# Performance work log

Hardware: AMD Instinct MI355X
Metric: run time of the kernel (lower is better)

The kernel has to match this reference:

```python
import jax, jax.numpy as jnp
import numpy as np

N_NODES = 100000
N_EDGES = 1600000
IN_FEATS = 128
HIDDEN = 128
OUT_FEATS = 64
N_GRAPHS = 64


def setup_inputs() -> dict:
    key = jax.random.key(0)
    ks = jax.random.split(key, 12)
    features = jax.random.normal(ks[0], (N_NODES, IN_FEATS), dtype=jnp.float32)
    src = jax.random.randint(ks[1], (N_EDGES,), 0, N_NODES, dtype=jnp.int32)
    dst = jax.random.randint(ks[2], (N_EDGES,), 0, N_NODES, dtype=jnp.int32)
    graph_ids = jnp.sort(jax.random.randint(ks[3], (N_NODES,), 0, N_GRAPHS, dtype=jnp.int32))
    s = 0.05
    W1 = jax.random.normal(ks[4], (IN_FEATS, HIDDEN), dtype=jnp.float32) * s
    b1 = jnp.zeros((HIDDEN,), jnp.float32)
    W2 = jax.random.normal(ks[5], (HIDDEN, HIDDEN), dtype=jnp.float32) * s
    b2 = jnp.zeros((HIDDEN,), jnp.float32)
    Wd1 = jax.random.normal(ks[6], (HIDDEN, HIDDEN), dtype=jnp.float32) * s
    bd1 = jnp.zeros((HIDDEN,), jnp.float32)
    Wd2 = jax.random.normal(ks[7], (HIDDEN, OUT_FEATS), dtype=jnp.float32) * s
    bd2 = jnp.zeros((OUT_FEATS,), jnp.float32)
    return {"features": features, "src": src, "dst": dst, "graph_ids": graph_ids,
            "W1": W1, "b1": b1, "W2": W2, "b2": b2,
            "Wd1": Wd1, "bd1": bd1, "Wd2": Wd2, "bd2": bd2}


def _gin_conv(x, src, dst, W, b):
    # DGL GINConv(aggregator='mean', eps=0): h = Linear((1+eps)*x + mean_{u->v} x_u)
    agg_sum = jax.ops.segment_sum(x[src], dst, num_segments=N_NODES)  # [N, d]
    deg = jax.ops.segment_sum(jnp.ones((src.shape[0],), x.dtype), dst, num_segments=N_NODES)  # [N]
    agg = jnp.where(deg[:, None] > 0, agg_sum / jnp.maximum(deg, 1.0)[:, None], 0.0)
    return (x + agg) @ W + b


def reference(features, src, dst, graph_ids, W1, b1, W2, b2, Wd1, bd1, Wd2, bd2):
    h = jax.nn.relu(_gin_conv(features, src, dst, W1, b1))
    h = jax.nn.relu(_gin_conv(h, src, dst, W2, b2))
    # dgl.mean_nodes: per-graph mean over nodes
    hg_sum = jax.ops.segment_sum(h, graph_ids, num_segments=N_GRAPHS)  # [G, H]
    counts = jax.ops.segment_sum(jnp.ones((h.shape[0],), h.dtype), graph_ids, num_segments=N_GRAPHS)
    hg = hg_sum / jnp.maximum(counts, 1.0)[:, None]
    reconstructed = jax.nn.relu(hg @ Wd1 + bd1) @ Wd2 + bd2
    return (hg, reconstructed)
```

## Files before the change

### kernel.cpp

```cpp
#include <hip/hip_runtime.h>

#define NN 100000
#define NE 1600000
#define FD 128
#define NG 64
#define OUTD 64
#define NBIN 391

typedef __attribute__((ext_vector_type(8))) short bf16x8;
typedef __attribute__((ext_vector_type(4))) float f32x4;
typedef __attribute__((ext_vector_type(2))) float f32x2;
typedef __attribute__((ext_vector_type(8))) unsigned short u16x8;

static __device__ __forceinline__ void atomAddF(float* p, float v) {
    __hip_atomic_fetch_add(p, v, __ATOMIC_RELAXED, __HIP_MEMORY_SCOPE_AGENT);
}
static __device__ __forceinline__ int atomAddI(int* p, int v) {
    return __hip_atomic_fetch_add(p, v, __ATOMIC_RELAXED, __HIP_MEMORY_SCOPE_AGENT);
}
static __device__ __forceinline__ unsigned short f2bf(float f) {
    unsigned int u = __float_as_uint(f);
    u += 0x7FFFu + ((u >> 16) & 1u);
    return (unsigned short)(u >> 16);
}
static __device__ __forceinline__ float bf2f(unsigned short h) {
    return __uint_as_float(((unsigned int)h) << 16);
}
static __device__ __forceinline__ unsigned char f2fp8(float v) {
    return (unsigned char)(__builtin_amdgcn_cvt_pk_fp8_f32(v, v, 0, false) & 0xff);
}

__global__ __launch_bounds__(256) void k_pre(
    const int* __restrict__ dst, const int* __restrict__ gid,
    int* __restrict__ bincnt, float* __restrict__ gcount,
    const float* __restrict__ W1, const float* __restrict__ W2,
    unsigned short* __restrict__ W1t, unsigned short* __restrict__ W2t,
    unsigned int* __restrict__ Y8dummy, unsigned int* __restrict__ Y82dummy)
{
    const int t = threadIdx.x;
    if (blockIdx.x < NBIN) {
        __shared__ int h[NBIN];
        for (int i = t; i < NBIN; i += 256) h[i] = 0;
        __syncthreads();
        int e0 = blockIdx.x * 4096;
        int e1 = min(e0 + 4096, NE);
        for (int e = e0 + t; e < e1; e += 256)
            atomicAdd(&h[dst[e] >> 8], 1);
        __syncthreads();
        for (int i = t; i < NBIN; i += 256)
            if (h[i]) atomAddI(&bincnt[i], h[i]);
    } else if (blockIdx.x < 2 * NBIN) {
        __shared__ float c[NG];
        if (t < NG) c[t] = 0.0f;
        __syncthreads();
        int i = (blockIdx.x - NBIN) * 256 + t;
        if (i < NN) atomicAdd(&c[gid[i]], 1.0f);
        __syncthreads();
        if (t < NG) {
            float v = c[t];
            if (v != 0.0f) atomAddF(&gcount[t], v);
        }
    } else {
        int idx = (blockIdx.x - 2 * NBIN) * 256 + t;
        if (idx < 32768) {
            const float* W = (idx < 16384) ? W1 : W2;
            unsigned short* Wt = (idx < 16384) ? W1t : W2t;
            int i = idx & 16383;
            int k = i >> 7, n = i & 127;
            Wt[n * 128 + k] = f2bf(W[i]);
        } else if (idx < 32768 + 32) {
            Y8dummy[idx - 32768] = 0;
        } else if (idx < 32768 + 64) {
            Y82dummy[idx - 32768 - 32] = 0;
        }
    }
}

__global__ void k_boff(const int* __restrict__ bincnt, int* __restrict__ pstart,
                       int* __restrict__ bcur) {
    __shared__ int s[512];
    int t = threadIdx.x;
    int v = (t < NBIN) ? bincnt[t] : 0;
    s[t] = v;
    __syncthreads();
    for (int d = 1; d < 512; d <<= 1) {
        int x = (t >= d) ? s[t - d] : 0;
        __syncthreads();
        s[t] += x;
        __syncthreads();
    }
    if (t < NBIN) {
        int p = s[t] - v;
        pstart[t] = p;
        bcur[t * 16] = p;
    }
}

static __device__ __forceinline__ void gemm_body(
    int base, const float* __restrict__ feat, const unsigned short* __restrict__ Wt,
    unsigned char* __restrict__ Y8)
{
    const int lane = threadIdx.x & 63;
    const int w = threadIdx.x >> 6;
    const int r = lane & 15;
    const int kb = lane >> 4;
    const int row = base + w * 16 + r;
    const bool rok = row < NN;

    bf16x8 a[4];
    #pragma unroll
    for (int kt = 0; kt < 4; ++kt) {
        float4 lo = {0,0,0,0}, hi = {0,0,0,0};
        if (rok) {
            const float4* p = reinterpret_cast<const float4*>(
                feat + (size_t)row * FD + kt * 32 + kb * 8);
            lo = p[0]; hi = p[1];
        }
        bf16x8 t;
        t[0] = (short)f2bf(lo.x); t[1] = (short)f2bf(lo.y);
        t[2] = (short)f2bf(lo.z); t[3] = (short)f2bf(lo.w);
        t[4] = (short)f2bf(hi.x); t[5] = (short)f2bf(hi.y);
        t[6] = (short)f2bf(hi.z); t[7] = (short)f2bf(hi.w);
        a[kt] = t;
    }

    f32x4 acc[8];
    #pragma unroll
    for (int ct = 0; ct < 8; ++ct) acc[ct] = (f32x4){0.f, 0.f, 0.f, 0.f};

    const int n = lane & 15;
    #pragma unroll
    for (int ct = 0; ct < 8; ++ct) {
        int col = ct * 16 + n;
        #pragma unroll
        for (int kt = 0; kt < 4; ++kt) {
            bf16x8 b = *reinterpret_cast<const bf16x8*>(
                Wt + (size_t)col * FD + kt * 32 + kb * 8);
            acc[ct] = __builtin_amdgcn_mfma_f32_16x16x32_bf16(a[kt], b, acc[ct], 0, 0, 0);
        }
    }

    const int rbase = base + w * 16 + (lane >> 4) * 4;
    #pragma unroll
    for (int reg = 0; reg < 4; ++reg) {
        int node = rbase + reg;
        if (node < NN) {
            #pragma unroll
            for (int ct = 0; ct < 8; ++ct)
                Y8[(size_t)node * FD + ct * 16 + n] = f2fp8(acc[ct][reg]);
        }
    }
}

__global__ __launch_bounds__(256) void k_mix(
    const int* __restrict__ src, const int* __restrict__ dst,
    int* __restrict__ bcur, unsigned int* __restrict__ pbuf,
    const float* __restrict__ feat, const unsigned short* __restrict__ Wt,
    unsigned char* __restrict__ Y8)
{
    int g = blockIdx.x;
    if (g % 5 == 0) {
        gemm_body((g / 5) * 64, feat, Wt, Y8);
    } else {
        int fb = g - g / 5 - 1;
        int e = fb * 256 + threadIdx.x;
        if (e < NE) {
            int d = dst[e];
            int b = d >> 8;
            int p = atomAddI(&bcur[b * 16], 1);
            pbuf[p] = ((unsigned int)(d & 255) << 17) | (unsigned int)src[e];
        }
    }
}

__global__ __launch_bounds__(256) void k_fill2(
    const unsigned int* __restrict__ pbuf, const int* __restrict__ pstart,
    const int* __restrict__ bcur, int* __restrict__ degi, int* __restrict__ off,
    int* __restrict__ eidx)
{
    __shared__ int ldeg[256], lpre[256], lcur[256];
    const int b = blockIdx.x;
    const int t = threadIdx.x;
    const int st = pstart[b];
    const int en = bcur[b * 16];
    const int cnt = en - st;

    ldeg[t] = 0;
    __syncthreads();
    for (int i = t; i < cnt; i += 256)
        atomicAdd(&ldeg[(int)(pbuf[st + i] >> 17)], 1);
    __syncthreads();

    const int d = ldeg[t];
    const int rd = (d + 7) & ~7;
    lpre[t] = rd;
    __syncthreads();
    for (int dd = 1; dd < 256; dd <<= 1) {
        int x = (t >= dd) ? lpre[t - dd] : 0;
        __syncthreads();
        lpre[t] += x;
        __syncthreads();
    }

    const int ebase = st + b * 2048;
    const int o = ebase + lpre[t] - rd;
    const int v = (b << 8) + t;
    if (v < NN) {
        degi[v] = d;
        off[v] = o;
        for (int j = d; j < rd; ++j) eidx[o + j] = NN;
    }
    lcur[t] = o;
    __syncthreads();

    for (int i = t; i < cnt; i += 256) {
        unsigned int pk = pbuf[st + i];
        int dl = (int)(pk >> 17);
        int s  = (int)(pk & 0x1FFFF);
        int p = atomicAdd(&lcur[dl], 1);
        eidx[p] = s;
    }
}

__global__ __launch_bounds__(256) void k_aggmm(
    const unsigned char* __restrict__ Y8, const int* __restrict__ off,
    const int* __restrict__ degi, const int* __restrict__ eidx,
    const float* __restrict__ bias, const unsigned short* __restrict__ Wt2,
    unsigned char* __restrict__ Y82)
{
    __shared__ unsigned short At[16 * FD];
    const int t = blockIdx.x * 256 + threadIdx.x;
    const int v = t >> 4;
    const int l = threadIdx.x & 15;
    const int gb = threadIdx.x & 48;
    const int e0 = off[v];
    const int d  = degi[v];
    const int pd = (d + 7) & ~7;

    float a[8];
    #pragma unroll
    for (int j = 0; j < 8; ++j) a[j] = 0.0f;

    const uint2* Y8v = reinterpret_cast<const uint2*>(Y8);
    const int eend = e0 + pd;
    for (int e = e0; e < eend; e += 8) {
        int myidx = eidx[e + (l & 7)];
        #pragma unroll
        for (int j = 0; j < 8; ++j) {
            int s = __shfl(myidx, gb + j, 64);
            uint2 q = Y8v[(size_t)s * 16 + l];
            f32x2 v0 = __builtin_amdgcn_cvt_pk_f32_fp8((int)q.x, false);
            f32x2 v1 = __builtin_amdgcn_cvt_pk_f32_fp8((int)q.x, true);
            f32x2 v2 = __builtin_amdgcn_cvt_pk_f32_fp8((int)q.y, false);
            f32x2 v3 = __builtin_amdgcn_cvt_pk_f32_fp8((int)q.y, true);
            a[0] += v0[0]; a[1] += v0[1]; a[2] += v1[0]; a[3] += v1[1];
            a[4] += v2[0]; a[5] += v2[1]; a[6] += v3[0]; a[7] += v3[1];
        }
    }

    const float inv = 1.0f / fmaxf((float)d, 1.0f);
    uint2 qs = Y8v[(size_t)v * 16 + l];
    f32x2 s0 = __builtin_amdgcn_cvt_pk_f32_fp8((int)qs.x, false);
    f32x2 s1 = __builtin_amdgcn_cvt_pk_f32_fp8((int)qs.x, true);
    f32x2 s2 = __builtin_amdgcn_cvt_pk_f32_fp8((int)qs.y, false);
    f32x2 s3 = __builtin_amdgcn_cvt_pk_f32_fp8((int)qs.y, true);
    float sf[8] = { s0[0], s0[1], s1[0], s1[1], s2[0], s2[1], s3[0], s3[1] };
    const float4* bp = reinterpret_cast<const float4*>(bias + l * 8);
    float4 b0 = bp[0], b1 = bp[1];
    const float* bb[8] = { &b0.x, &b0.y, &b0.z, &b0.w, &b1.x, &b1.y, &b1.z, &b1.w };

    {
        u16x8 o;
        #pragma unroll
        for (int j = 0; j < 8; ++j)
            o[j] = f2bf(fmaxf(sf[j] + a[j] * inv + *bb[j], 0.0f));
        int g = threadIdx.x >> 4;
        char* AtB = reinterpret_cast<char*>(At);
        *reinterpret_cast<u16x8*>(AtB + g * 256 + ((l * 16) ^ ((g & 7) << 4))) = o;
    }
    __syncthreads();

    {
        const int lane = threadIdx.x & 63;
        const int w = threadIdx.x >> 6;
        const int r = lane & 15;
        const int kb = lane >> 4;
        const int n = lane & 15;
        char* AtB = reinterpret_cast<char*>(At);

        bf16x8 af[4];
        #pragma unroll
        for (int kt = 0; kt < 4; ++kt)
            af[kt] = *reinterpret_cast<bf16x8*>(
                AtB + r * 256 + ((kt * 64 + kb * 16) ^ ((r & 7) << 4)));

        f32x4 acc[2];
        acc[0] = (f32x4){0.f, 0.f, 0.f, 0.f};
        acc[1] = (f32x4){0.f, 0.f, 0.f, 0.f};
        #pragma unroll
        for (int ct = 0; ct < 2; ++ct) {
            int col = w * 32 + ct * 16 + n;
            #pragma unroll
            for (int kt = 0; kt < 4; ++kt) {
                bf16x8 bf = *reinterpret_cast<const bf16x8*>(
                    Wt2 + (size_t)col * FD + kt * 32 + kb * 8);
                acc[ct] = __builtin_amdgcn_mfma_f32_16x16x32_bf16(af[kt], bf, acc[ct], 0, 0, 0);
            }
        }

        const int nb = blockIdx.x * 16 + (lane >> 4) * 4;
        #pragma unroll
        for (int reg = 0; reg < 4; ++reg) {
            #pragma unroll
            for (int ct = 0; ct < 2; ++ct)
                Y82[(size_t)(nb + reg) * FD + w * 32 + ct * 16 + n] = f2fp8(acc[ct][reg]);
        }
    }
}

__global__ __launch_bounds__(256) void k_aggp(
    const unsigned char* __restrict__ Y82, const int* __restrict__ off,
    const int* __restrict__ degi, const int* __restrict__ eidx,
    const float* __restrict__ bias,
    const int* __restrict__ gid, float* __restrict__ hg_sum)
{
    __shared__ float hl[FD];
    if (threadIdx.x < FD) hl[threadIdx.x] = 0.0f;
    int gid0 = gid[blockIdx.x * 16];
    __syncthreads();

    const int t = blockIdx.x * 256 + threadIdx.x;
    const int v = t >> 4;
    const int l = threadIdx.x & 15;
    const int gb = threadIdx.x & 48;
    const int e0 = off[v];
    const int d  = degi[v];
    const int pd = (d + 7) & ~7;

    float a[8];
    #pragma unroll
    for (int j = 0; j < 8; ++j) a[j] = 0.0f;

    const uint2* Y8v = reinterpret_cast<const uint2*>(Y82);
    const int eend = e0 + pd;
    for (int e = e0; e < eend; e += 8) {
        int myidx = eidx[e + (l & 7)];
        #pragma unroll
        for (int j = 0; j < 8; ++j) {
            int s = __shfl(myidx, gb + j, 64);
            uint2 q = Y8v[(size_t)s * 16 + l];
            f32x2 v0 = __builtin_amdgcn_cvt_pk_f32_fp8((int)q.x, false);
            f32x2 v1 = __builtin_amdgcn_cvt_pk_f32_fp8((int)q.x, true);
            f32x2 v2 = __builtin_amdgcn_cvt_pk_f32_fp8((int)q.y, false);
            f32x2 v3 = __builtin_amdgcn_cvt_pk_f32_fp8((int)q.y, true);
            a[0] += v0[0]; a[1] += v0[1]; a[2] += v1[0]; a[3] += v1[1];
            a[4] += v2[0]; a[5] += v2[1]; a[6] += v3[0]; a[7] += v3[1];
        }
    }

    const float inv = 1.0f / fmaxf((float)d, 1.0f);
    uint2 qs = Y8v[(size_t)v * 16 + l];
    f32x2 s0 = __builtin_amdgcn_cvt_pk_f32_fp8((int)qs.x, false);
    f32x2 s1 = __builtin_amdgcn_cvt_pk_f32_fp8((int)qs.x, true);
    f32x2 s2 = __builtin_amdgcn_cvt_pk_f32_fp8((int)qs.y, false);
    f32x2 s3 = __builtin_amdgcn_cvt_pk_f32_fp8((int)qs.y, true);
    float sf[8] = { s0[0], s0[1], s1[0], s1[1], s2[0], s2[1], s3[0], s3[1] };
    const float4* bp = reinterpret_cast<const float4*>(bias + l * 8);
    float4 b0 = bp[0], b1 = bp[1];
    const float* bb[8] = { &b0.x, &b0.y, &b0.z, &b0.w, &b1.x, &b1.y, &b1.z, &b1.w };

    float hv[8];
    #pragma unroll
    for (int j = 0; j < 8; ++j)
        hv[j] = fmaxf(sf[j] + a[j] * inv + *bb[j], 0.0f);

    int g = gid[v];
    int fo = l * 8;
    if (g == gid0) {
        #pragma unroll
        for (int j = 0; j < 8; ++j) atomicAdd(&hl[fo + j], hv[j]);
    } else {
        #pragma unroll
        for (int j = 0; j < 8; ++j) atomAddF(&hg_sum[(size_t)g * FD + fo + j], hv[j]);
    }
    __syncthreads();
    if (threadIdx.x < FD)
        atomAddF(&hg_sum[(size_t)gid0 * FD + threadIdx.x], hl[threadIdx.x]);
}

__global__ __launch_bounds__(128) void k_dec(
    const float* __restrict__ hg_sum, const float* __restrict__ gcount,
    const float* __restrict__ Wd1, const float* __restrict__ bd1,
    const float* __restrict__ Wd2, const float* __restrict__ bd2,
    float* __restrict__ out)
{
    __shared__ float hgL[FD];
    __shared__ float t1L[FD];
    const int g = blockIdx.x;
    const int t = threadIdx.x;
    const float invc = 1.0f / fmaxf(gcount[g], 1.0f);

    float v = hg_sum[(size_t)g * FD + t] * invc;
    hgL[t] = v;
    out[(size_t)g * FD + t] = v;
    __syncthreads();

    float acc = bd1[t];
    #pragma unroll 8
    for (int k = 0; k < FD; ++k)
        acc += hgL[k] * Wd1[k * FD + t];
    t1L[t] = fmaxf(acc, 0.0f);
    __syncthreads();

    if (t < OUTD) {
        float acc2 = bd2[t];
        #pragma unroll 8
        for (int k = 0; k < FD; ++k)
            acc2 += t1L[k] * Wd2[k * OUTD + t];
        out[NG * FD + (size_t)g * OUTD + t] = acc2;
    }
}

extern "C" void kernel_launch(void* const* d_in, const int* in_sizes, int n_in,
                              void* d_out, int out_size, void* d_ws, size_t ws_size,
                              hipStream_t stream) {
    const float* feat = (const float*)d_in[0];
    const int*   src  = (const int*)d_in[1];
    const int*   dst  = (const int*)d_in[2];
    const int*   gid  = (const int*)d_in[3];
    const float* W1   = (const float*)d_in[4];
    const float* b1   = (const float*)d_in[5];
    const float* W2   = (const float*)d_in[6];
    const float* b2   = (const float*)d_in[7];
    const float* Wd1  = (const float*)d_in[8];
    const float* bd1  = (const float*)d_in[9];
    const float* Wd2  = (const float*)d_in[10];
    const float* bd2  = (const float*)d_in[11];
    float* out = (float*)d_out;

    char* wsb = (char*)d_ws;
    int*   bincnt = (int*)wsb;
    float* gcount = (float*)(wsb + 512ll * 4);
    float* hg_sum = (float*)(wsb + 576ll * 4);
    int*   pstart = (int*)(wsb + 8768ll * 4);
    int*   bcur   = (int*)(wsb + 9280ll * 4);
    int*   degi   = (int*)(wsb + 15536ll * 4);
    int*   off    = (int*)(wsb + 115536ll * 4);
    int*   eidx   = (int*)(wsb + 215536ll * 4);
    unsigned int* pbuf = (unsigned int*)(wsb + 2616336ll * 4);
    unsigned short* W1t = (unsigned short*)(wsb + 4216336ll * 4);
    unsigned short* W2t = (unsigned short*)(wsb + 4224528ll * 4);
    unsigned char*  Y8  = (unsigned char*)(wsb + 4232720ll * 4);
    unsigned char*  Y82 = (unsigned char*)(wsb + 7432752ll * 4);

    hipMemsetAsync(d_ws, 0, (size_t)8768 * 4, stream);

    k_pre<<<2 * NBIN + 129, 256, 0, stream>>>(dst, gid, bincnt, gcount, W1, W2,
                                              W1t, W2t,
                                              (unsigned int*)(Y8 + (size_t)NN * FD),
                                              (unsigned int*)(Y82 + (size_t)NN * FD));
    k_boff<<<1, 512, 0, stream>>>(bincnt, pstart, bcur);
    k_mix<<<7815, 256, 0, stream>>>(src, dst, bcur, pbuf, feat, W1t, Y8);
    k_fill2<<<NBIN, 256, 0, stream>>>(pbuf, pstart, bcur, degi, off, eidx);
    k_aggmm<<<NN / 16, 256, 0, stream>>>(Y8, off, degi, eidx, b1, W2t, Y82);
    k_aggp<<<NN / 16, 256, 0, stream>>>(Y82, off, degi, eidx, b2, gid, hg_sum);
    k_dec<<<NG, 128, 0, stream>>>(hg_sum, gcount, Wd1, bd1, Wd2, bd2, out);
}
```

Measured before the change: 294.5 us.

## Batch 16 gather loads per step, pad CSR to 16, partition edge scatter by bin

The aggregation loops now read 16 neighbor indices at once and issue all 16 fp8 row loads before converting any of them, so more memory requests are in flight. CSR rows are padded to multiples of 16 to match, which enlarges the eidx region and shifts the workspace offsets. The edge-binning stage in k_mix now puts its GEMM blocks first and launches 8 passes over the edges, each handling only the bins of one residue class mod 8, to spread atomic contention on bin counters. The cost is reading dst eight times, more padding work in the gathers, and higher register pressure.

```diff
diff --git a/kernel.cpp b/kernel.cpp
--- a/kernel.cpp
+++ b/kernel.cpp
@@ -6,6 +6,7 @@
 #define NG 64
 #define OUTD 64
 #define NBIN 391
+#define NGEMM1 1563
 
 typedef __attribute__((ext_vector_type(8))) short bf16x8;
 typedef __attribute__((ext_vector_type(4))) float f32x4;
@@ -22,9 +23,6 @@
     unsigned int u = __float_as_uint(f);
     u += 0x7FFFu + ((u >> 16) & 1u);
     return (unsigned short)(u >> 16);
-}
-static __device__ __forceinline__ float bf2f(unsigned short h) {
-    return __uint_as_float(((unsigned int)h) << 16);
 }
 static __device__ __forceinline__ unsigned char f2fp8(float v) {
     return (unsigned char)(__builtin_amdgcn_cvt_pk_fp8_f32(v, v, 0, false) & 0xff);
@@ -159,16 +157,20 @@
     unsigned char* __restrict__ Y8)
 {
     int g = blockIdx.x;
-    if (g % 5 == 0) {
-        gemm_body((g / 5) * 64, feat, Wt, Y8);
+    if (g < NGEMM1) {
+        gemm_body(g * 64, feat, Wt, Y8);
     } else {
-        int fb = g - g / 5 - 1;
-        int e = fb * 256 + threadIdx.x;
+        int fb = g - NGEMM1;
+        int c  = fb >> 3;
+        int xg = (fb + 3) & 7;
+        int e = c * 256 + threadIdx.x;
         if (e < NE) {
             int d = dst[e];
             int b = d >> 8;
-            int p = atomAddI(&bcur[b * 16], 1);
-            pbuf[p] = ((unsigned int)(d & 255) << 17) | (unsigned int)src[e];
+            if ((b & 7) == xg) {
+                int p = atomAddI(&bcur[b * 16], 1);
+                pbuf[p] = ((unsigned int)(d & 255) << 17) | (unsigned int)src[e];
+            }
         }
     }
 }
@@ -192,7 +194,7 @@
     __syncthreads();
 
     const int d = ldeg[t];
-    const int rd = (d + 7) & ~7;
+    const int rd = (d + 15) & ~15;
     lpre[t] = rd;
     __syncthreads();
     for (int dd = 1; dd < 256; dd <<= 1) {
@@ -202,7 +204,7 @@
         __syncthreads();
     }
 
-    const int ebase = st + b * 2048;
+    const int ebase = st + b * 4096;
     const int o = ebase + lpre[t] - rd;
     const int v = (b << 8) + t;
     if (v < NN) {
@@ -219,6 +221,30 @@
         int s  = (int)(pk & 0x1FFFF);
         int p = atomicAdd(&lcur[dl], 1);
         eidx[p] = s;
+    }
+}
+
+static __device__ __forceinline__ void gather16(
+    const uint2* __restrict__ Y8v, const int* __restrict__ eidx,
+    int e0, int eend, int l, int gb, float* a)
+{
+    for (int e = e0; e < eend; e += 16) {
+        int my = eidx[e + l];
+        uint2 q[16];
+        #pragma unroll
+        for (int j = 0; j < 16; ++j) {
+            int s = __shfl(my, gb + j, 64);
+            q[j] = Y8v[(size_t)s * 16 + l];
+        }
+        #pragma unroll
+        for (int j = 0; j < 16; ++j) {
+            f32x2 v0 = __builtin_amdgcn_cvt_pk_f32_fp8((int)q[j].x, false);
+            f32x2 v1 = __builtin_amdgcn_cvt_pk_f32_fp8((int)q[j].x, true);
+            f32x2 v2 = __builtin_amdgcn_cvt_pk_f32_fp8((int)q[j].y, false);
+            f32x2 v3 = __builtin_amdgcn_cvt_pk_f32_fp8((int)q[j].y, true);
+            a[0] += v0[0]; a[1] += v0[1]; a[2] += v1[0]; a[3] += v1[1];
+            a[4] += v2[0]; a[5] += v2[1]; a[6] += v3[0]; a[7] += v3[1];
+        }
     }
 }
 
@@ -235,28 +261,14 @@
     const int gb = threadIdx.x & 48;
     const int e0 = off[v];
     const int d  = degi[v];
-    const int pd = (d + 7) & ~7;
+    const int pd = (d + 15) & ~15;
 
     float a[8];
     #pragma unroll
     for (int j = 0; j < 8; ++j) a[j] = 0.0f;
 
     const uint2* Y8v = reinterpret_cast<const uint2*>(Y8);
-    const int eend = e0 + pd;
-    for (int e = e0; e < eend; e += 8) {
-        int myidx = eidx[e + (l & 7)];
-        #pragma unroll
-        for (int j = 0; j < 8; ++j) {
-            int s = __shfl(myidx, gb + j, 64);
-            uint2 q = Y8v[(size_t)s * 16 + l];
-            f32x2 v0 = __builtin_amdgcn_cvt_pk_f32_fp8((int)q.x, false);
-            f32x2 v1 = __builtin_amdgcn_cvt_pk_f32_fp8((int)q.x, true);
-            f32x2 v2 = __builtin_amdgcn_cvt_pk_f32_fp8((int)q.y, false);
-            f32x2 v3 = __builtin_amdgcn_cvt_pk_f32_fp8((int)q.y, true);
-            a[0] += v0[0]; a[1] += v0[1]; a[2] += v1[0]; a[3] += v1[1];
-            a[4] += v2[0]; a[5] += v2[1]; a[6] += v3[0]; a[7] += v3[1];
-        }
-    }
+    gather16(Y8v, eidx, e0, e0 + pd, l, gb, a);
 
     const float inv = 1.0f / fmaxf((float)d, 1.0f);
     uint2 qs = Y8v[(size_t)v * 16 + l];
@@ -335,28 +347,14 @@
     const int gb = threadIdx.x & 48;
     const int e0 = off[v];
     const int d  = degi[v];
-    const int pd = (d + 7) & ~7;
+    const int pd = (d + 15) & ~15;
 
     float a[8];
     #pragma unroll
     for (int j = 0; j < 8; ++j) a[j] = 0.0f;
 
     const uint2* Y8v = reinterpret_cast<const uint2*>(Y82);
-    const int eend = e0 + pd;
-    for (int e = e0; e < eend; e += 8) {
-        int myidx = eidx[e + (l & 7)];
-        #pragma unroll
-        for (int j = 0; j < 8; ++j) {
-            int s = __shfl(myidx, gb + j, 64);
-            uint2 q = Y8v[(size_t)s * 16 + l];
-            f32x2 v0 = __builtin_amdgcn_cvt_pk_f32_fp8((int)q.x, false);
-            f32x2 v1 = __builtin_amdgcn_cvt_pk_f32_fp8((int)q.x, true);
-            f32x2 v2 = __builtin_amdgcn_cvt_pk_f32_fp8((int)q.y, false);
-            f32x2 v3 = __builtin_amdgcn_cvt_pk_f32_fp8((int)q.y, true);
-            a[0] += v0[0]; a[1] += v0[1]; a[2] += v1[0]; a[3] += v1[1];
-            a[4] += v2[0]; a[5] += v2[1]; a[6] += v3[0]; a[7] += v3[1];
-        }
-    }
+    gather16(Y8v, eidx, e0, e0 + pd, l, gb, a);
 
     const float inv = 1.0f / fmaxf((float)d, 1.0f);
     uint2 qs = Y8v[(size_t)v * 16 + l];
@@ -447,11 +445,11 @@
     int*   degi   = (int*)(wsb + 15536ll * 4);
     int*   off    = (int*)(wsb + 115536ll * 4);
     int*   eidx   = (int*)(wsb + 215536ll * 4);
-    unsigned int* pbuf = (unsigned int*)(wsb + 2616336ll * 4);
-    unsigned short* W1t = (unsigned short*)(wsb + 4216336ll * 4);
-    unsigned short* W2t = (unsigned short*)(wsb + 4224528ll * 4);
-    unsigned char*  Y8  = (unsigned char*)(wsb + 4232720ll * 4);
-    unsigned char*  Y82 = (unsigned char*)(wsb + 7432752ll * 4);
+    unsigned int* pbuf = (unsigned int*)(wsb + 3425536ll * 4);
+    unsigned short* W1t = (unsigned short*)(wsb + 5025536ll * 4);
+    unsigned short* W2t = (unsigned short*)(wsb + 5033728ll * 4);
+    unsigned char*  Y8  = (unsigned char*)(wsb + 5041920ll * 4);
+    unsigned char*  Y82 = (unsigned char*)(wsb + 8245152ll * 4);
 
     hipMemsetAsync(d_ws, 0, (size_t)8768 * 4, stream);
 
@@ -460,7 +458,7 @@
                                               (unsigned int*)(Y8 + (size_t)NN * FD),
                                               (unsigned int*)(Y82 + (size_t)NN * FD));
     k_boff<<<1, 512, 0, stream>>>(bincnt, pstart, bcur);
-    k_mix<<<7815, 256, 0, stream>>>(src, dst, bcur, pbuf, feat, W1t, Y8);
+    k_mix<<<NGEMM1 + 50000, 256, 0, stream>>>(src, dst, bcur, pbuf, feat, W1t, Y8);
     k_fill2<<<NBIN, 256, 0, stream>>>(pbuf, pstart, bcur, degi, off, eidx);
     k_aggmm<<<NN / 16, 256, 0, stream>>>(Y8, off, degi, eidx, b1, W2t, Y82);
     k_aggp<<<NN / 16, 256, 0, stream>>>(Y82, off, degi, eidx, b2, gid, hg_sum);
```

After: 323.9 us. +10.0%, slower.

## Aggregate edge binning atomics per block via shared-memory histogram in k_mix

Applied to the files above, without the earlier changes.

The edge-partitioning part of k_mix now has each block process 4096 edges. It builds a local shared-memory histogram of destination bins and reserves space with one global atomic per bin, then scatters edges using shared-memory atomics. This replaces one global atomic per edge with about 391 global atomics per block. The block schedule also changes from interleaving gemm and fill blocks 1:4 to placing all 391 fill blocks first and the 1563 gemm blocks after. Each fill block reads dst twice and now has more serial work per block.

```diff
diff --git a/kernel.cpp b/kernel.cpp
--- a/kernel.cpp
+++ b/kernel.cpp
@@ -6,6 +6,8 @@
 #define NG 64
 #define OUTD 64
 #define NBIN 391
+#define NGFILL 391
+#define NGEMM1 1563
 
 typedef __attribute__((ext_vector_type(8))) short bf16x8;
 typedef __attribute__((ext_vector_type(4))) float f32x4;
@@ -22,9 +24,6 @@
     unsigned int u = __float_as_uint(f);
     u += 0x7FFFu + ((u >> 16) & 1u);
     return (unsigned short)(u >> 16);
-}
-static __device__ __forceinline__ float bf2f(unsigned short h) {
-    return __uint_as_float(((unsigned int)h) << 16);
 }
 static __device__ __forceinline__ unsigned char f2fp8(float v) {
     return (unsigned char)(__builtin_amdgcn_cvt_pk_fp8_f32(v, v, 0, false) & 0xff);
@@ -159,15 +158,28 @@
     unsigned char* __restrict__ Y8)
 {
     int g = blockIdx.x;
-    if (g % 5 == 0) {
-        gemm_body((g / 5) * 64, feat, Wt, Y8);
+    if (g >= NGFILL) {
+        gemm_body((g - NGFILL) * 64, feat, Wt, Y8);
     } else {
-        int fb = g - g / 5 - 1;
-        int e = fb * 256 + threadIdx.x;
-        if (e < NE) {
+        __shared__ int h[NBIN];
+        __shared__ int lcur[NBIN];
+        const int t = threadIdx.x;
+        const int e0 = g * 4096;
+        const int e1 = min(e0 + 4096, NE);
+
+        for (int i = t; i < NBIN; i += 256) h[i] = 0;
+        __syncthreads();
+        for (int e = e0 + t; e < e1; e += 256)
+            atomicAdd(&h[dst[e] >> 8], 1);
+        __syncthreads();
+        for (int i = t; i < NBIN; i += 256) {
+            int c = h[i];
+            lcur[i] = c ? atomAddI(&bcur[i * 16], c) : 0;
+        }
+        __syncthreads();
+        for (int e = e0 + t; e < e1; e += 256) {
             int d = dst[e];
-            int b = d >> 8;
-            int p = atomAddI(&bcur[b * 16], 1);
+            int p = atomicAdd(&lcur[d >> 8], 1);
             pbuf[p] = ((unsigned int)(d & 255) << 17) | (unsigned int)src[e];
         }
     }
@@ -460,7 +472,7 @@
                                               (unsigned int*)(Y8 + (size_t)NN * FD),
                                               (unsigned int*)(Y82 + (size_t)NN * FD));
     k_boff<<<1, 512, 0, stream>>>(bincnt, pstart, bcur);
-    k_mix<<<7815, 256, 0, stream>>>(src, dst, bcur, pbuf, feat, W1t, Y8);
+    k_mix<<<NGFILL + NGEMM1, 256, 0, stream>>>(src, dst, bcur, pbuf, feat, W1t, Y8);
     k_fill2<<<NBIN, 256, 0, stream>>>(pbuf, pstart, bcur, degi, off, eidx);
     k_aggmm<<<NN / 16, 256, 0, stream>>>(Y8, off, degi, eidx, b1, W2t, Y82);
     k_aggp<<<NN / 16, 256, 0, stream>>>(Y82, off, degi, eidx, b2, gid, hg_sum);
```

Measured after the change: 254.5 us, median of 2. -13.6%, faster.
